# Kernel optimization log

Hardware: AMD Instinct MI355X
Metric: run time of the kernel (lower is better)

## Reference

```python
import jax, jax.numpy as jnp
import numpy as np

N_NODES = 100000


def gcn_conv(x, edge_index, W, b, n_nodes):
    # PyG GCNConv: add self-loops, symmetric normalization, linear, scatter-add, bias.
    src, dst = edge_index[0], edge_index[1]
    loop = jnp.arange(n_nodes, dtype=edge_index.dtype)
    src = jnp.concatenate([src, loop])  # [E + N]
    dst = jnp.concatenate([dst, loop])
    # degree of target nodes (edge weight = 1)
    deg = jax.ops.segment_sum(jnp.ones_like(dst, dtype=x.dtype), dst,
                              num_segments=n_nodes)
    dinv = jnp.where(deg > 0, jax.lax.rsqrt(deg), 0.0)
    norm = dinv[src] * dinv[dst]  # [E + N]
    h = x @ W  # [N, out] small dense GEMM
    msg = h[src] * norm[:, None]  # gather + scale (memory-bound)
    out = jax.ops.segment_sum(msg, dst, num_segments=n_nodes)
    return out + b


def setup_inputs() -> dict:
    key = jax.random.key(0)
    k = jax.random.split(key, 6)
    n, e = N_NODES, 1600000
    d_in, d_hid, d_out = 128, 128, 64
    x = jax.random.normal(k[0], (n, d_in), dtype=jnp.float32)
    edge_index = jax.random.randint(k[1], (2, e), 0, n, dtype=jnp.int64)
    W1 = jax.random.normal(k[2], (d_in, d_hid), dtype=jnp.float32) / np.sqrt(d_in)
    b1 = jnp.zeros((d_hid,), dtype=jnp.float32)
    W2 = jax.random.normal(k[3], (d_hid, d_out), dtype=jnp.float32) / np.sqrt(d_hid)
    b2 = jnp.zeros((d_out,), dtype=jnp.float32)
    return {"x": x, "edge_index": edge_index, "W1": W1, "b1": b1,
            "W2": W2, "b2": b2}


def reference(x, edge_index, W1, b1, W2, b2):
    n = x.shape[0]
    h = gcn_conv(x, edge_index, W1, b1, n)
    h = jax.nn.relu(h)
    return gcn_conv(h, edge_index, W2, b2, n)
```

## Files before the change

### kernel.cpp

```cpp
#include <hip/hip_runtime.h>

typedef __attribute__((ext_vector_type(8))) short bf16x8;
typedef __attribute__((ext_vector_type(4))) float f32x4;

#define NBINS 391
#define NBLK  196
#define ECHUNK 8192
#define BKTPAD 1024


__device__ __forceinline__ unsigned short f2bf(float f) {
    unsigned u = __float_as_uint(f);
    u += 0x7fffu + ((u >> 16) & 1u);
    return (unsigned short)(u >> 16);
}
__device__ __forceinline__ float bf_lo(unsigned u) { return __uint_as_float(u << 16); }
__device__ __forceinline__ float bf_hi(unsigned u) { return __uint_as_float(u & 0xffff0000u); }

__device__ __forceinline__ void acc8(float* a, uint4 u) {
    a[0] += bf_lo(u.x); a[1] += bf_hi(u.x);
    a[2] += bf_lo(u.y); a[3] += bf_hi(u.y);
    a[4] += bf_lo(u.z); a[5] += bf_hi(u.z);
    a[6] += bf_lo(u.w); a[7] += bf_hi(u.w);
}
__device__ __forceinline__ void acc4(float* a, uint2 u) {
    a[0] += bf_lo(u.x); a[1] += bf_hi(u.x);
    a[2] += bf_lo(u.y); a[3] += bf_hi(u.y);
}


__global__ __launch_bounds__(256) void bucket_hist(const int* __restrict__ ei, int E, int n,
                                                   int* __restrict__ hist_t) {
    __shared__ int h[NBINS];
    int t = threadIdx.x, blk = blockIdx.x;
    for (int i = t; i < NBINS; i += 256) h[i] = 0;
    __syncthreads();
    int start = blk * ECHUNK;
    int end = min(E, start + ECHUNK);
    for (int i = start + t; i < end; i += 256) {
        int s = ei[i];
        int d = ei[E + i];
        if ((unsigned)d < (unsigned)n && (unsigned)s < (unsigned)n)
            atomicAdd(&h[d >> 8], 1);
    }
    __syncthreads();
    for (int i = t; i < NBINS; i += 256) hist_t[i * NBLK + blk] = h[i];
}

__global__ __launch_bounds__(256) void scan_partial(const int* __restrict__ in,
                                                    int ntot, int* __restrict__ blocksum) {
    int base = blockIdx.x * 1024;
    int t = threadIdx.x;
    int s = 0;
#pragma unroll
    for (int j = 0; j < 4; ++j) {
        int i = base + (t << 2) + j;
        if (i < ntot) s += in[i];
    }
#pragma unroll
    for (int off = 1; off < 64; off <<= 1) s += __shfl_xor(s, off);
    __shared__ int ws[4];
    if ((t & 63) == 0) ws[t >> 6] = s;
    __syncthreads();
    if (t == 0) blocksum[blockIdx.x] = ws[0] + ws[1] + ws[2] + ws[3];
}

__global__ __launch_bounds__(256) void scan_blocksums(int* __restrict__ blocksum, int nb) {
    __shared__ int sh[256];
    int t = threadIdx.x;
    sh[t] = (t < nb) ? blocksum[t] : 0;
    __syncthreads();
#pragma unroll
    for (int off = 1; off < 256; off <<= 1) {
        int v = (t >= off) ? sh[t - off] : 0;
        __syncthreads();
        sh[t] += v;
        __syncthreads();
    }
    if (t < nb) blocksum[t] = (t == 0) ? 0 : sh[t - 1];
}

__global__ __launch_bounds__(256) void scan2_final(const int* __restrict__ in,
                                                   const int* __restrict__ blockoff,
                                                   int ntot, int* __restrict__ out) {
    int base = blockIdx.x * 1024;
    int t = threadIdx.x;
    int v[4];
    int s = 0;
#pragma unroll
    for (int j = 0; j < 4; ++j) {
        int i = base + (t << 2) + j;
        v[j] = (i < ntot) ? in[i] : 0;
        s += v[j];
    }
    __shared__ int sh[256];
    sh[t] = s;
    __syncthreads();
#pragma unroll
    for (int off = 1; off < 256; off <<= 1) {
        int x = (t >= off) ? sh[t - off] : 0;
        __syncthreads();
        sh[t] += x;
        __syncthreads();
    }
    int run = blockoff[blockIdx.x] + (sh[t] - s);
#pragma unroll
    for (int j = 0; j < 4; ++j) {
        int i = base + (t << 2) + j;
        if (i < ntot) {
            out[i] = run;
            run += v[j];
        }
    }
    int lo = base + (t << 2);
    if (lo <= ntot - 1 && ntot - 1 < lo + 4) out[ntot] = run;
}

__global__ __launch_bounds__(256) void bucket_scatter(const int* __restrict__ ei, int E, int n,
                                                      const int* __restrict__ off,
                                                      unsigned long long* __restrict__ ebuf) {
    __shared__ int lo[NBINS];
    int t = threadIdx.x, blk = blockIdx.x;
    for (int i = t; i < NBINS; i += 256) lo[i] = off[i * NBLK + blk];
    __syncthreads();
    int start = blk * ECHUNK;
    int end = min(E, start + ECHUNK);
    for (int i = start + t; i < end; i += 256) {
        int s = ei[i];
        int d = ei[E + i];
        if ((unsigned)d < (unsigned)n && (unsigned)s < (unsigned)n) {
            int pos = atomicAdd(&lo[d >> 8], 1);
            if (pos < E) ebuf[pos] = ((unsigned long long)(unsigned)d << 32) | (unsigned)s;
        }
    }
}

__global__ __launch_bounds__(256) void bucket_csr(const unsigned long long* __restrict__ ebuf,
                                                  const int* __restrict__ off, int E, int n,
                                                  int* __restrict__ rowptr,
                                                  int* __restrict__ rend,
                                                  float* __restrict__ dinv,
                                                  int* __restrict__ srcs) {
    int b = blockIdx.x;
    int t = threadIdx.x;
    int bstart = off[b * NBLK];
    int bend = off[(b + 1) * NBLK];
    int pstart = bstart + b * BKTPAD;
    __shared__ int cnt[256], sh[256], basev[256], fill[256];
    cnt[t] = 0;
    __syncthreads();
    for (int i = bstart + t; i < bend; i += 256) {
        int d = (int)(ebuf[i] >> 32);
        atomicAdd(&cnt[d & 255], 1);
    }
    __syncthreads();
    int myc = cnt[t];
    int pmyc = (myc + 3) & ~3;
    sh[t] = pmyc;
    __syncthreads();
#pragma unroll
    for (int o = 1; o < 256; o <<= 1) {
        int v = (t >= o) ? sh[t - o] : 0;
        __syncthreads();
        sh[t] += v;
        __syncthreads();
    }
    int pincl = sh[t];
    int pbase = pstart + pincl - pmyc;
    basev[t] = pbase;
    fill[t] = 0;
    int d = b * 256 + t;
    if (d < n) {
        rowptr[d] = pbase;
        rend[d] = pbase + pmyc;
        dinv[d] = rsqrtf((float)(myc + 1));
        for (int r = myc; r < pmyc; ++r) srcs[pbase + r] = n;
    }
    __syncthreads();
    for (int i = bstart + t; i < bend; i += 256) {
        unsigned long long p = ebuf[i];
        int dl = (int)(p >> 32) & 255;
        int s = (int)(p & 0xffffffffu);
        int r = atomicAdd(&fill[dl], 1);
        srcs[basev[dl] + r] = s;
    }
}


__global__ __launch_bounds__(256) void prep_w(const float* __restrict__ W1,
                                              const float* __restrict__ W2,
                                              unsigned short* __restrict__ Wt1,
                                              unsigned short* __restrict__ Wt2,
                                              unsigned short* __restrict__ g1,
                                              unsigned short* __restrict__ g2, int n) {
    int t = blockIdx.x * blockDim.x + threadIdx.x;
    if (t < 128 * 128) {
        int k = t >> 7, c = t & 127;
        Wt1[c * 128 + k] = f2bf(W1[t]);
    } else if (t < 128 * 128 + 128 * 64) {
        int i = t - 128 * 128;
        int k = i >> 6, c = i & 63;
        Wt2[c * 128 + k] = f2bf(W2[i]);
    } else if (t < 128 * 128 + 128 * 64 + 128) {
        g1[(size_t)n * 128 + (t - 128 * 128 - 128 * 64)] = 0;
    } else if (t < 128 * 128 + 128 * 64 + 192) {
        g2[(size_t)n * 64 + (t - 128 * 128 - 128 * 64 - 128)] = 0;
    }
}


template <int M, bool IN_BF16>
__global__ __launch_bounds__(256) void gemm_mfma(const void* __restrict__ Xv,
                                                 const unsigned short* __restrict__ Wt,
                                                 const float* __restrict__ dinv,
                                                 unsigned short* __restrict__ G16,
                                                 int n, int ntiles) {
    constexpr int K = 128;
    constexpr int BM = 64;
    __shared__ unsigned short Xs[BM * K];
    __shared__ unsigned short Wl[M * K];
    int t = threadIdx.x;

#pragma unroll
    for (int i = 0; i < M / 16; ++i) {
        int f = t + i * 256;
        int c = f >> 4, k8 = f & 15;
        uint4 v = ((const uint4*)Wt)[f];
        int addr = (c * 256 + k8 * 16) ^ ((c & 7) << 4);
        *(uint4*)((char*)Wl + addr) = v;
    }

    int w = t >> 6, l = t & 63;
    int lg = l >> 4, lm = l & 15;
    constexpr int NCT = M / 16;
    union F8 { uint2 u2[2]; bf16x8 v; };

    for (int tile = blockIdx.x; tile < ntiles; tile += gridDim.x) {
        int blockRow = tile * BM;
        __syncthreads();

        if (!IN_BF16) {
            const float* X = (const float*)Xv;
#pragma unroll
            for (int i = 0; i < 8; ++i) {
                int f = t + i * 256;
                int m = f >> 5, k4 = f & 31;
                float4 v = make_float4(0.f, 0.f, 0.f, 0.f);
                if (blockRow + m < n) v = ((const float4*)(X + (size_t)(blockRow + m) * K))[k4];
                uint2 p;
                p.x = (unsigned)f2bf(v.x) | ((unsigned)f2bf(v.y) << 16);
                p.y = (unsigned)f2bf(v.z) | ((unsigned)f2bf(v.w) << 16);
                int addr = (m * 256 + k4 * 8) ^ ((m & 7) << 4);
                *(uint2*)((char*)Xs + addr) = p;
            }
        } else {
            const unsigned short* X = (const unsigned short*)Xv;
#pragma unroll
            for (int i = 0; i < 4; ++i) {
                int f = t + i * 256;
                int m = f >> 4, k8 = f & 15;
                uint4 v = make_uint4(0u, 0u, 0u, 0u);
                if (blockRow + m < n) v = ((const uint4*)(X + (size_t)(blockRow + m) * K))[k8];
                int addr = (m * 256 + k8 * 16) ^ ((m & 7) << 4);
                *(uint4*)((char*)Xs + addr) = v;
            }
        }
        __syncthreads();

        bf16x8 afr[4];
        int mrow = 16 * w + lm;
        int swa = (mrow & 7) << 4;
#pragma unroll
        for (int kk = 0; kk < 4; ++kk) {
            int pa = mrow * 256 + (32 * kk + 4 * lg) * 2;
            F8 a;
            a.u2[0] = *(const uint2*)((const char*)Xs + (pa ^ swa));
            a.u2[1] = *(const uint2*)((const char*)Xs + ((pa + 32) ^ swa));
            afr[kk] = a.v;
        }

        f32x4 acc[NCT];
#pragma unroll
        for (int ct = 0; ct < NCT; ++ct) acc[ct] = (f32x4){0.f, 0.f, 0.f, 0.f};

#pragma unroll
        for (int ct = 0; ct < NCT; ++ct) {
            int c = ct * 16 + lm;
            int swc = (c & 7) << 4;
#pragma unroll
            for (int kk = 0; kk < 4; ++kk) {
                int pb = c * 256 + (32 * kk + 4 * lg) * 2;
                F8 b;
                b.u2[0] = *(const uint2*)((const char*)Wl + (pb ^ swc));
                b.u2[1] = *(const uint2*)((const char*)Wl + ((pb + 32) ^ swc));
                acc[ct] = __builtin_amdgcn_mfma_f32_16x16x32_bf16(afr[kk], b.v, acc[ct], 0, 0, 0);
            }
        }

        float dv[4];
#pragma unroll
        for (int q = 0; q < 4; ++q) {
            int r = blockRow + 16 * w + 4 * lg + q;
            dv[q] = (r < n) ? dinv[r] : 0.f;
        }
#pragma unroll
        for (int ct = 0; ct < NCT; ++ct) {
#pragma unroll
            for (int q = 0; q < 4; ++q) {
                int r = blockRow + 16 * w + 4 * lg + q;
                if (r < n) G16[(size_t)r * M + ct * 16 + lm] = f2bf(acc[ct][q] * dv[q]);
            }
        }
    }
}


__global__ __launch_bounds__(256) void agg_d128(const unsigned short* __restrict__ G16,
                                                const int* __restrict__ srcs,
                                                const int* __restrict__ rowptr,
                                                const int* __restrict__ rend,
                                                const float* __restrict__ dinv,
                                                const float* __restrict__ bias,
                                                unsigned short* __restrict__ out, int n) {
    int wid = (blockIdx.x * blockDim.x + threadIdx.x) >> 6;
    int lane = threadIdx.x & 63;
    if (wid >= n) return;
    int g = lane >> 4;
    int lh = lane & 15;

    float acc[8];
    {
        uint4 u = make_uint4(0u, 0u, 0u, 0u);
        if (g == 0) u = ((const uint4*)G16)[(size_t)wid * 16 + lh];
        acc[0] = bf_lo(u.x); acc[1] = bf_hi(u.x);
        acc[2] = bf_lo(u.y); acc[3] = bf_hi(u.y);
        acc[4] = bf_lo(u.z); acc[5] = bf_hi(u.z);
        acc[6] = bf_lo(u.w); acc[7] = bf_hi(u.w);
    }

    int beg = rowptr[wid], end = rend[wid];
    for (int base = beg; base < end; base += 64) {
        int mm = end - base;
        if (mm > 64) mm = 64;
        int sv = (base + lane < end) ? srcs[base + lane] : n;
        int j = 0;
        for (; j + 8 <= mm; j += 8) {
            int s0 = __shfl(sv, j + g);
            int s1 = __shfl(sv, j + 4 + g);
            uint4 u0 = ((const uint4*)G16)[(size_t)s0 * 16 + lh];
            uint4 u1 = ((const uint4*)G16)[(size_t)s1 * 16 + lh];
            acc8(acc, u0);
            acc8(acc, u1);
        }
        if (j < mm) {
            int s0 = __shfl(sv, j + g);
            uint4 u0 = ((const uint4*)G16)[(size_t)s0 * 16 + lh];
            acc8(acc, u0);
        }
    }

#pragma unroll
    for (int k = 0; k < 8; ++k) {
        acc[k] += __shfl_xor(acc[k], 16);
        acc[k] += __shfl_xor(acc[k], 32);
    }

    if (g == 0) {
        float di = dinv[wid];
        float4 b0 = ((const float4*)bias)[2 * lh];
        float4 b1 = ((const float4*)bias)[2 * lh + 1];
        float o[8];
        o[0] = fmaxf(acc[0] * di + b0.x, 0.f);
        o[1] = fmaxf(acc[1] * di + b0.y, 0.f);
        o[2] = fmaxf(acc[2] * di + b0.z, 0.f);
        o[3] = fmaxf(acc[3] * di + b0.w, 0.f);
        o[4] = fmaxf(acc[4] * di + b1.x, 0.f);
        o[5] = fmaxf(acc[5] * di + b1.y, 0.f);
        o[6] = fmaxf(acc[6] * di + b1.z, 0.f);
        o[7] = fmaxf(acc[7] * di + b1.w, 0.f);
        uint4 p;
        p.x = (unsigned)f2bf(o[0]) | ((unsigned)f2bf(o[1]) << 16);
        p.y = (unsigned)f2bf(o[2]) | ((unsigned)f2bf(o[3]) << 16);
        p.z = (unsigned)f2bf(o[4]) | ((unsigned)f2bf(o[5]) << 16);
        p.w = (unsigned)f2bf(o[6]) | ((unsigned)f2bf(o[7]) << 16);
        ((uint4*)(out + (size_t)wid * 128))[lh] = p;
    }
}

__global__ __launch_bounds__(256) void agg_d64(const unsigned short* __restrict__ G16,
                                               const int* __restrict__ srcs,
                                               const int* __restrict__ rowptr,
                                               const int* __restrict__ rend,
                                               const float* __restrict__ dinv,
                                               const float* __restrict__ bias,
                                               float* __restrict__ out, int n) {
    int wid = (blockIdx.x * blockDim.x + threadIdx.x) >> 6;
    int lane = threadIdx.x & 63;
    if (wid >= n) return;
    int g = lane >> 4;
    int lh = lane & 15;

    float acc[4];
    {
        uint2 u = make_uint2(0u, 0u);
        if (g == 0) u = ((const uint2*)G16)[(size_t)wid * 16 + lh];
        acc[0] = bf_lo(u.x); acc[1] = bf_hi(u.x);
        acc[2] = bf_lo(u.y); acc[3] = bf_hi(u.y);
    }

    int beg = rowptr[wid], end = rend[wid];
    for (int base = beg; base < end; base += 64) {
        int mm = end - base;
        if (mm > 64) mm = 64;
        int sv = (base + lane < end) ? srcs[base + lane] : n;
        int j = 0;
        for (; j + 8 <= mm; j += 8) {
            int s0 = __shfl(sv, j + g);
            int s1 = __shfl(sv, j + 4 + g);
            uint2 u0 = ((const uint2*)G16)[(size_t)s0 * 16 + lh];
            uint2 u1 = ((const uint2*)G16)[(size_t)s1 * 16 + lh];
            acc4(acc, u0);
            acc4(acc, u1);
        }
        if (j < mm) {
            int s0 = __shfl(sv, j + g);
            uint2 u0 = ((const uint2*)G16)[(size_t)s0 * 16 + lh];
            acc4(acc, u0);
        }
    }

#pragma unroll
    for (int k = 0; k < 4; ++k) {
        acc[k] += __shfl_xor(acc[k], 16);
        acc[k] += __shfl_xor(acc[k], 32);
    }

    if (g == 0) {
        float di = dinv[wid];
        float4 b = ((const float4*)bias)[lh];
        float4 o;
        o.x = acc[0] * di + b.x;
        o.y = acc[1] * di + b.y;
        o.z = acc[2] * di + b.z;
        o.w = acc[3] * di + b.w;
        ((float4*)(out + (size_t)wid * 64))[lh] = o;
    }
}


extern "C" void kernel_launch(void* const* d_in, const int* in_sizes, int n_in,
                              void* d_out, int out_size, void* d_ws, size_t ws_size,
                              hipStream_t stream) {
    const float* x = (const float*)d_in[0];
    const int* ei = (const int*)d_in[1];
    const float* W1 = (const float*)d_in[2];
    const float* b1 = (const float*)d_in[3];
    const float* W2 = (const float*)d_in[4];
    const float* b2 = (const float*)d_in[5];
    float* out = (float*)d_out;

    const int n = in_sizes[0] / 128;
    const int E = in_sizes[1] / 2;
    const int ntot = NBINS * NBLK;

    char* ws = (char*)d_ws;
    size_t off_b = 0;
    auto alloc = [&](size_t bytes) {
        void* p = ws + off_b;
        off_b = (off_b + bytes + 255) & ~(size_t)255;
        return p;
    };
    unsigned short* g1 = (unsigned short*)alloc(((size_t)n + 1) * 128 * 2);
    unsigned short* g2 = (unsigned short*)alloc(((size_t)n + 1) * 64 * 2);
    unsigned short* a1 = (unsigned short*)alloc((size_t)n * 128 * 2);
    int* rowptr = (int*)alloc((size_t)n * 4);
    int* rend = (int*)alloc((size_t)n * 4);
    float* dinv = (float*)alloc((size_t)n * 4);
    int* srcs = (int*)alloc(((size_t)E + (size_t)NBINS * BKTPAD) * 4);
    unsigned long long* ebuf = (unsigned long long*)alloc((size_t)E * 8);
    int* hist_t = (int*)alloc((size_t)ntot * 4);
    int* off = (int*)alloc(((size_t)ntot + 1) * 4);
    int* blocksum = (int*)alloc(1024 * 4);
    unsigned short* Wt1 = (unsigned short*)alloc(128 * 128 * 2);
    unsigned short* Wt2 = (unsigned short*)alloc(64 * 128 * 2);

    const int nb_scan = (ntot + 1023) / 1024;
    const int ntiles = (n + 63) / 64;
    const int gb = 768;

    prep_w<<<97, 256, 0, stream>>>(W1, W2, Wt1, Wt2, g1, g2, n);
    bucket_hist<<<NBLK, 256, 0, stream>>>(ei, E, n, hist_t);
    scan_partial<<<nb_scan, 256, 0, stream>>>(hist_t, ntot, blocksum);
    scan_blocksums<<<1, 256, 0, stream>>>(blocksum, nb_scan);
    scan2_final<<<nb_scan, 256, 0, stream>>>(hist_t, blocksum, ntot, off);
    bucket_scatter<<<NBLK, 256, 0, stream>>>(ei, E, n, off, ebuf);
    bucket_csr<<<NBINS, 256, 0, stream>>>(ebuf, off, E, n, rowptr, rend, dinv, srcs);

    gemm_mfma<128, false><<<gb, 256, 0, stream>>>(x, Wt1, dinv, g1, n, ntiles);
    agg_d128<<<(n + 3) / 4, 256, 0, stream>>>(g1, srcs, rowptr, rend, dinv, b1, a1, n);

    gemm_mfma<64, true><<<gb, 256, 0, stream>>>(a1, Wt2, dinv, g2, n, ntiles);
    agg_d64<<<(n + 3) / 4, 256, 0, stream>>>(g2, srcs, rowptr, rend, dinv, b2, out, n);
}
```

Before: 213.3 us.

## Widen d64 gather to uint4 lanes, deepen unroll, smaller edge chunks

The d64 aggregation kernel now has each lane load 16 bytes (8 lanes per 128-byte row, 8 edges in flight per wave) instead of 8 bytes, with an extra shuffle-reduce level. The d128 aggregation loop is unrolled to issue four gathers per iteration. The bucket kernels use 4096-edge chunks over 391 blocks, and the histogram no longer reads the source index. Out-of-range sources are clamped to n instead of being dropped. The aim is more memory-level parallelism and fewer load instructions, at the cost of more registers, a longer reduction, and a larger per-block histogram table.

```diff
diff --git a/kernel.cpp b/kernel.cpp
--- a/kernel.cpp
+++ b/kernel.cpp
@@ -4,8 +4,8 @@
 typedef __attribute__((ext_vector_type(4))) float f32x4;
 
 #define NBINS 391
-#define NBLK  196
-#define ECHUNK 8192
+#define ECHUNK 4096
+#define NBLK  391
 #define BKTPAD 1024
 
 
@@ -23,10 +23,6 @@
     a[4] += bf_lo(u.z); a[5] += bf_hi(u.z);
     a[6] += bf_lo(u.w); a[7] += bf_hi(u.w);
 }
-__device__ __forceinline__ void acc4(float* a, uint2 u) {
-    a[0] += bf_lo(u.x); a[1] += bf_hi(u.x);
-    a[2] += bf_lo(u.y); a[3] += bf_hi(u.y);
-}
 
 
 __global__ __launch_bounds__(256) void bucket_hist(const int* __restrict__ ei, int E, int n,
@@ -38,10 +34,8 @@
     int start = blk * ECHUNK;
     int end = min(E, start + ECHUNK);
     for (int i = start + t; i < end; i += 256) {
-        int s = ei[i];
         int d = ei[E + i];
-        if ((unsigned)d < (unsigned)n && (unsigned)s < (unsigned)n)
-            atomicAdd(&h[d >> 8], 1);
+        if ((unsigned)d < (unsigned)n) atomicAdd(&h[d >> 8], 1);
     }
     __syncthreads();
     for (int i = t; i < NBINS; i += 256) hist_t[i * NBLK + blk] = h[i];
@@ -128,7 +122,8 @@
     for (int i = start + t; i < end; i += 256) {
         int s = ei[i];
         int d = ei[E + i];
-        if ((unsigned)d < (unsigned)n && (unsigned)s < (unsigned)n) {
+        if ((unsigned)d < (unsigned)n) {
+            if ((unsigned)s > (unsigned)n) s = n;
             int pos = atomicAdd(&lo[d >> 8], 1);
             if (pos < E) ebuf[pos] = ((unsigned long long)(unsigned)d << 32) | (unsigned)s;
         }
@@ -344,15 +339,18 @@
         if (mm > 64) mm = 64;
         int sv = (base + lane < end) ? srcs[base + lane] : n;
         int j = 0;
-        for (; j + 8 <= mm; j += 8) {
+        for (; j + 16 <= mm; j += 16) {
             int s0 = __shfl(sv, j + g);
             int s1 = __shfl(sv, j + 4 + g);
+            int s2 = __shfl(sv, j + 8 + g);
+            int s3 = __shfl(sv, j + 12 + g);
             uint4 u0 = ((const uint4*)G16)[(size_t)s0 * 16 + lh];
             uint4 u1 = ((const uint4*)G16)[(size_t)s1 * 16 + lh];
-            acc8(acc, u0);
-            acc8(acc, u1);
-        }
-        if (j < mm) {
+            uint4 u2 = ((const uint4*)G16)[(size_t)s2 * 16 + lh];
+            uint4 u3 = ((const uint4*)G16)[(size_t)s3 * 16 + lh];
+            acc8(acc, u0); acc8(acc, u1); acc8(acc, u2); acc8(acc, u3);
+        }
+        for (; j < mm; j += 4) {
             int s0 = __shfl(sv, j + g);
             uint4 u0 = ((const uint4*)G16)[(size_t)s0 * 16 + lh];
             acc8(acc, u0);
@@ -397,15 +395,17 @@
     int wid = (blockIdx.x * blockDim.x + threadIdx.x) >> 6;
     int lane = threadIdx.x & 63;
     if (wid >= n) return;
-    int g = lane >> 4;
-    int lh = lane & 15;
-
-    float acc[4];
+    int g = lane >> 3;
+    int lh = lane & 7;
+
+    float acc[8];
     {
-        uint2 u = make_uint2(0u, 0u);
-        if (g == 0) u = ((const uint2*)G16)[(size_t)wid * 16 + lh];
+        uint4 u = make_uint4(0u, 0u, 0u, 0u);
+        if (g == 0) u = ((const uint4*)G16)[(size_t)wid * 8 + lh];
         acc[0] = bf_lo(u.x); acc[1] = bf_hi(u.x);
         acc[2] = bf_lo(u.y); acc[3] = bf_hi(u.y);
+        acc[4] = bf_lo(u.z); acc[5] = bf_hi(u.z);
+        acc[6] = bf_lo(u.w); acc[7] = bf_hi(u.w);
     }
 
     int beg = rowptr[wid], end = rend[wid];
@@ -414,36 +414,42 @@
         if (mm > 64) mm = 64;
         int sv = (base + lane < end) ? srcs[base + lane] : n;
         int j = 0;
-        for (; j + 8 <= mm; j += 8) {
+        for (; j + 16 <= mm; j += 16) {
             int s0 = __shfl(sv, j + g);
-            int s1 = __shfl(sv, j + 4 + g);
-            uint2 u0 = ((const uint2*)G16)[(size_t)s0 * 16 + lh];
-            uint2 u1 = ((const uint2*)G16)[(size_t)s1 * 16 + lh];
-            acc4(acc, u0);
-            acc4(acc, u1);
-        }
-        if (j < mm) {
+            int s1 = __shfl(sv, j + 8 + g);
+            uint4 u0 = ((const uint4*)G16)[(size_t)s0 * 8 + lh];
+            uint4 u1 = ((const uint4*)G16)[(size_t)s1 * 8 + lh];
+            acc8(acc, u0); acc8(acc, u1);
+        }
+        for (; j < mm; j += 8) {
             int s0 = __shfl(sv, j + g);
-            uint2 u0 = ((const uint2*)G16)[(size_t)s0 * 16 + lh];
-            acc4(acc, u0);
-        }
-    }
-
-#pragma unroll
-    for (int k = 0; k < 4; ++k) {
+            uint4 u0 = ((const uint4*)G16)[(size_t)s0 * 8 + lh];
+            acc8(acc, u0);
+        }
+    }
+
+#pragma unroll
+    for (int k = 0; k < 8; ++k) {
+        acc[k] += __shfl_xor(acc[k], 8);
         acc[k] += __shfl_xor(acc[k], 16);
         acc[k] += __shfl_xor(acc[k], 32);
     }
 
     if (g == 0) {
         float di = dinv[wid];
-        float4 b = ((const float4*)bias)[lh];
-        float4 o;
-        o.x = acc[0] * di + b.x;
-        o.y = acc[1] * di + b.y;
-        o.z = acc[2] * di + b.z;
-        o.w = acc[3] * di + b.w;
-        ((float4*)(out + (size_t)wid * 64))[lh] = o;
+        float4 b0 = ((const float4*)bias)[2 * lh];
+        float4 b1 = ((const float4*)bias)[2 * lh + 1];
+        float4 o0, o1;
+        o0.x = acc[0] * di + b0.x;
+        o0.y = acc[1] * di + b0.y;
+        o0.z = acc[2] * di + b0.z;
+        o0.w = acc[3] * di + b0.w;
+        o1.x = acc[4] * di + b1.x;
+        o1.y = acc[5] * di + b1.y;
+        o1.z = acc[6] * di + b1.z;
+        o1.w = acc[7] * di + b1.w;
+        ((float4*)(out + (size_t)wid * 64))[2 * lh] = o0;
+        ((float4*)(out + (size_t)wid * 64))[2 * lh + 1] = o1;
     }
 }
 
```

After: 201.1 us. 5.7% less time.
